# Kernel optimization log

Hardware: AMD Instinct MI355X
Metric: run time of the kernel (lower is better)

The kernel has to match this reference:

```python
import jax, jax.numpy as jnp
import numpy as np

EPS = 1e-12

def _l2_normalize(v, axis):
    norm = jnp.linalg.norm(v, ord=2, axis=axis, keepdims=True)
    return v / jnp.maximum(norm, EPS)

def setup_inputs() -> dict:
    key = jax.random.key(0)
    k1, k2, k3 = jax.random.split(key, 3)
    B, H, W, D, K = 16, 56, 56, 512, 32
    x = jax.random.normal(k1, (B, H, W, D), dtype=jnp.float32)
    # 1x1 conv weight (no bias): equivalent to a (D,K) matmul; he_normal-ish scale
    Wc = jax.random.normal(k2, (D, K), dtype=jnp.float32) * jnp.sqrt(2.0 / D)
    # cluster centers, original shape (1,1,1,512,32) -> stored as (D,K)
    C = jax.random.normal(k3, (D, K), dtype=jnp.float32) * jnp.sqrt(2.0 / D)
    return {"x": x, "Wc": Wc, "C": C}

def reference(x, Wc, C):
    # soft-assignment: 1x1 conv + softmax over clusters
    s = jnp.einsum('bhwd,dk->bhwk', x, Wc)          # (B,H,W,K)
    a = jax.nn.softmax(s, axis=-1)                   # (B,H,W,K)
    # v[b,d,k] = sum_{h,w} a[b,h,w,k] * (x[b,h,w,d] + C[d,k])
    #          = einsum(a,x) + C * sum_{h,w} a   (avoids (B,H,W,D,K) intermediate)
    ax = jnp.einsum('bhwk,bhwd->bdk', a, x)          # (B,D,K)
    a_sum = jnp.sum(a, axis=(1, 2))                  # (B,K)
    v = ax + C[None, :, :] * a_sum[:, None, :]       # (B,D,K)
    # intra-normalize over cluster axis (dim=2), flatten, L2 normalize
    v = _l2_normalize(v, axis=2)
    v = v.reshape(v.shape[0], -1)                    # (B, D*K)
    return _l2_normalize(v, axis=1)
```

## Files before the change

kernel.cpp:

```cpp
#include <hip/hip_runtime.h>
#include <math.h>


#define BATCH 16
#define HW    3136
#define DIM   512
#define KCL   32
#define NCHK  49
#define SLABF (BATCH * DIM * KCL + 256)

typedef __attribute__((ext_vector_type(8))) short short8;
typedef __attribute__((ext_vector_type(4))) float f32x4;

__device__ __forceinline__ void atomAddF(float* p, float v) {
    unsafeAtomicAdd(p, v);
}

__device__ __forceinline__ unsigned short f2bf(float f) {
    unsigned u = __float_as_uint(f);
    return (unsigned short)((u + 0x7FFFu + ((u >> 16) & 1u)) >> 16);
}

__device__ __forceinline__ short8 pack_frag(float4 lo, float4 hi) {
    union { unsigned short h[8]; short8 s; } r;
    r.h[0] = f2bf(lo.x); r.h[1] = f2bf(lo.y); r.h[2] = f2bf(lo.z); r.h[3] = f2bf(lo.w);
    r.h[4] = f2bf(hi.x); r.h[5] = f2bf(hi.y); r.h[6] = f2bf(hi.z); r.h[7] = f2bf(hi.w);
    return r.s;
}

#define WT_STR 520
#define AT_STR 72
#define XT_STR 72

#define LOAD_PF(PF, DC)                                                        \
    _Pragma("unroll")                                                          \
    for (int i = 0; i < 8; ++i) {                                              \
        const int p = (ph + 2 * i) * 4;                                        \
        _Pragma("unroll")                                                      \
        for (int j = 0; j < 4; ++j)                                            \
            PF[i * 4 + j] = xc[(size_t)(p + j) * DIM + (DC)];                  \
    }

#define P2_STAGE(PF)                                                           \
    _Pragma("unroll")                                                          \
    for (int i = 0; i < 8; ++i) {                                              \
        const int p = (ph + 2 * i) * 4;                                        \
        ushort4 w;                                                             \
        w.x = f2bf(PF[i * 4 + 0]); w.y = f2bf(PF[i * 4 + 1]);                  \
        w.z = f2bf(PF[i * 4 + 2]); w.w = f2bf(PF[i * 4 + 3]);                  \
        *(ushort4*)&xt[xtrow * XT_STR + (p ^ xsw)] = w;                        \
    }

#define P2_MFMA_STORE(DC)                                                      \
    {                                                                          \
        f32x4 z = {0.f, 0.f, 0.f, 0.f};                                        \
        f32x4 pacc[2][2];                                                      \
        pacc[0][0] = z; pacc[0][1] = z; pacc[1][0] = z; pacc[1][1] = z;        \
        _Pragma("unroll")                                                      \
        for (int s_ = 0; s_ < 2; ++s_) {                                       \
            const int pb = s_ * 32 + quad * 8;                                 \
            short8 bf0 = *(const short8*)&aT[l15 * AT_STR + pb];               \
            short8 bf1 = *(const short8*)&aT[(16 + l15) * AT_STR + pb];        \
            _Pragma("unroll")                                                  \
            for (int m2 = 0; m2 < 2; ++m2) {                                   \
                const int dloc = wv * 32 + m2 * 16 + l15;                      \
                short8 af = *(const short8*)&xt[dloc * XT_STR + (pb ^ (((dloc >> 3) & 7) << 3))]; \
                pacc[m2][0] = __builtin_amdgcn_mfma_f32_16x16x32_bf16(af, bf0, pacc[m2][0], 0, 0, 0); \
                pacc[m2][1] = __builtin_amdgcn_mfma_f32_16x16x32_bf16(af, bf1, pacc[m2][1], 0, 0, 0); \
            }                                                                  \
        }                                                                      \
        _Pragma("unroll")                                                      \
        for (int m2 = 0; m2 < 2; ++m2) {                                       \
            const int dr = (DC) + (wv * 2 + m2) * 16 + quad * 4;               \
            _Pragma("unroll")                                                  \
            for (int r = 0; r < 4; ++r) {                                      \
                vp[(size_t)(dr + r) * KCL + l15]      = pacc[m2][0][r];        \
                vp[(size_t)(dr + r) * KCL + 16 + l15] = pacc[m2][1][r];        \
            }                                                                  \
        }                                                                      \
    }

__global__ __launch_bounds__(256, 3) void k_sax(const float* __restrict__ x,
                                                const float* __restrict__ Wc,
                                                float* __restrict__ vpart,
                                                float* __restrict__ a_sum) {
    __shared__ __align__(16) unsigned short wt[32 * WT_STR];
    __shared__ __align__(16) unsigned short aT[KCL * AT_STR];
    __shared__ float asum_l[4][32];
    const int t    = threadIdx.x;
    const int lane = t & 63;
    const int wv   = t >> 6;
    const int l15  = lane & 15;
    const int quad = lane >> 4;
    const int n0   = blockIdx.x * 64;
    const int b    = n0 / HW;
    const int ch   = blockIdx.x % NCHK;

    const float* xr = x + (size_t)(n0 + wv * 16 + l15) * DIM + quad * 8;

    float4 afb[2][2];
#pragma unroll
    for (int c = 0; c < 2; ++c) {
        afb[c][0] = *(const float4*)(xr + c * 32);
        afb[c][1] = *(const float4*)(xr + c * 32 + 4);
    }

#pragma unroll
    for (int i = 0; i < 16; ++i) {
        int f  = i * 256 + t;
        int d  = f >> 3;
        int k4 = (f & 7) * 4;
        float4 v = *(const float4*)(Wc + (size_t)d * KCL + k4);
        wt[(k4 + 0) * WT_STR + d] = f2bf(v.x);
        wt[(k4 + 1) * WT_STR + d] = f2bf(v.y);
        wt[(k4 + 2) * WT_STR + d] = f2bf(v.z);
        wt[(k4 + 3) * WT_STR + d] = f2bf(v.w);
    }
    __syncthreads();

    f32x4 acc0 = {0.f, 0.f, 0.f, 0.f};
    f32x4 acc1 = {0.f, 0.f, 0.f, 0.f};
#pragma unroll
    for (int c = 0; c < 16; ++c) {
        float4 lo = afb[c & 1][0], hi = afb[c & 1][1];
        if (c < 14) {
            afb[c & 1][0] = *(const float4*)(xr + (c + 2) * 32);
            afb[c & 1][1] = *(const float4*)(xr + (c + 2) * 32 + 4);
        }
        short8 af = pack_frag(lo, hi);
        short8 b0 = *(const short8*)&wt[l15 * WT_STR + c * 32 + quad * 8];
        short8 b1 = *(const short8*)&wt[(16 + l15) * WT_STR + c * 32 + quad * 8];
        acc0 = __builtin_amdgcn_mfma_f32_16x16x32_bf16(af, b0, acc0, 0, 0, 0);
        acc1 = __builtin_amdgcn_mfma_f32_16x16x32_bf16(af, b1, acc1, 0, 0, 0);
    }

    float at0 = 0.f, at1 = 0.f;
#pragma unroll
    for (int r = 0; r < 4; ++r) {
        float m = fmaxf(acc0[r], acc1[r]);
        m = fmaxf(m, __shfl_xor(m, 1));
        m = fmaxf(m, __shfl_xor(m, 2));
        m = fmaxf(m, __shfl_xor(m, 4));
        m = fmaxf(m, __shfl_xor(m, 8));
        float e0 = __expf(acc0[r] - m);
        float e1 = __expf(acc1[r] - m);
        float s = e0 + e1;
        s += __shfl_xor(s, 1);
        s += __shfl_xor(s, 2);
        s += __shfl_xor(s, 4);
        s += __shfl_xor(s, 8);
        float inv = 1.f / s;
        float a0 = e0 * inv, a1 = e1 * inv;
        const int pos = wv * 16 + quad * 4 + r;
        aT[l15 * AT_STR + pos]        = f2bf(a0);
        aT[(16 + l15) * AT_STR + pos] = f2bf(a1);
        at0 += a0; at1 += a1;
    }
    at0 += __shfl_xor(at0, 16); at0 += __shfl_xor(at0, 32);
    at1 += __shfl_xor(at1, 16); at1 += __shfl_xor(at1, 32);
    if (quad == 0) {
        asum_l[wv][l15]      = at0;
        asum_l[wv][16 + l15] = at1;
    }

    const int rw    = lane & 31;
    const int ph    = lane >> 5;
    const int xtrow = wv * 32 + rw;
    const int xsw   = ((xtrow >> 3) & 7) << 3;
    unsigned short* xt = wt;
    const float* xc = x + (size_t)n0 * DIM + xtrow;
    float* vp = vpart + (size_t)ch * SLABF + (size_t)b * DIM * KCL;

    float pfA[32], pfB[32];
    LOAD_PF(pfA, 0);

    __syncthreads();
    if (t < 32)
        atomAddF(&a_sum[b * KCL + t],
                 asum_l[0][t] + asum_l[1][t] + asum_l[2][t] + asum_l[3][t]);

    LOAD_PF(pfB, 128);

    P2_STAGE(pfA);
    __syncthreads();
    LOAD_PF(pfA, 256);
    P2_MFMA_STORE(0);
    P2_STAGE(pfB);
    __syncthreads();
    LOAD_PF(pfB, 384);
    P2_MFMA_STORE(128);
    P2_STAGE(pfA);
    __syncthreads();
    P2_MFMA_STORE(256);
    P2_STAGE(pfB);
    __syncthreads();
    P2_MFMA_STORE(384);
}

__global__ __launch_bounds__(256) void k_norm1(const float* __restrict__ vpart,
                                               const float* __restrict__ a_sum,
                                               const float* __restrict__ Cc,
                                               float* __restrict__ out,
                                               float* __restrict__ ssq) {
    const int t = threadIdx.x;
    const int row = blockIdx.x * 8 + (t >> 5);
    const int k = t & 31;
    const int b = row >> 9;
    const int d = row & 511;

    const float* vp = vpart + (size_t)row * KCL + k;
    float s0 = 0.f, s1 = 0.f, s2 = 0.f, s3 = 0.f;
#pragma unroll
    for (int ps = 0; ps < 48; ps += 4) {
        s0 += vp[(size_t)(ps + 0) * SLABF];
        s1 += vp[(size_t)(ps + 1) * SLABF];
        s2 += vp[(size_t)(ps + 2) * SLABF];
        s3 += vp[(size_t)(ps + 3) * SLABF];
    }
    s0 += vp[(size_t)48 * SLABF];
    float v = (s0 + s1) + (s2 + s3) + Cc[d * KCL + k] * a_sum[b * KCL + k];

    float ss = v * v;
    ss += __shfl_xor(ss, 1, 32);  ss += __shfl_xor(ss, 2, 32);
    ss += __shfl_xor(ss, 4, 32);  ss += __shfl_xor(ss, 8, 32);
    ss += __shfl_xor(ss, 16, 32);
    float inv = 1.f / fmaxf(sqrtf(ss), 1e-12f);
    float r = v * inv;
    out[(size_t)row * KCL + k] = r;

    float bs = r * r;
    for (int off = 32; off > 0; off >>= 1) bs += __shfl_down(bs, off, 64);
    __shared__ float red[4];
    if ((t & 63) == 0) red[t >> 6] = bs;
    __syncthreads();
    if (t == 0) atomAddF(&ssq[b], (red[0] + red[1]) + (red[2] + red[3]));
}

__global__ __launch_bounds__(256) void k_norm2(float* __restrict__ out,
                                               const float* __restrict__ ssq) {
    const int i4 = blockIdx.x * 256 + threadIdx.x;
    const int b = i4 >> 12;
    float inv = 1.f / fmaxf(sqrtf(ssq[b]), 1e-12f);
    float4 v = *(float4*)(out + (size_t)i4 * 4);
    v.x *= inv; v.y *= inv; v.z *= inv; v.w *= inv;
    *(float4*)(out + (size_t)i4 * 4) = v;
}

extern "C" void kernel_launch(void* const* d_in, const int* in_sizes, int n_in,
                              void* d_out, int out_size, void* d_ws, size_t ws_size,
                              hipStream_t stream) {
    const float* x  = (const float*)d_in[0];
    const float* Wc = (const float*)d_in[1];
    const float* Cc = (const float*)d_in[2];
    float* out = (float*)d_out;

    char* ws = (char*)d_ws;
    float* vpart = (float*)ws;
    float* a_sum = (float*)(ws + (size_t)NCHK * SLABF * 4);
    float* ssq   = (float*)(ws + (size_t)NCHK * SLABF * 4 + 2048);

    hipMemsetAsync(a_sum, 0, 2048 + 64, stream);

    k_sax  <<<784, 256, 0, stream>>>(x, Wc, vpart, a_sum);
    k_norm1<<<1024, 256, 0, stream>>>(vpart, a_sum, Cc, out, ssq);
    k_norm2<<<256, 256, 0, stream>>>(out, ssq);
}
```

Before: 198.2 us.

## Deepen x prefetch with asm loads and explicit vmcnt waits, drop phase-2 barriers

Phase 1 now issues eight chunks of x loads up front through inline-asm global loads. It consumes them with explicitly counted vmcnt waits, so memory latency overlaps the MFMA chain. Phase 2 drops its block-wide barriers between the staging and MFMA steps and uses explicit vmcnt waits to keep more prefetched loads in flight. The a_sum atomic moves to the end of the kernel. The deeper prefetch raises register pressure. Removing the barriers is only safe if each wave reads back only the shared-memory rows it wrote itself.

```diff
diff --git a/kernel.cpp b/kernel.cpp
--- a/kernel.cpp
+++ b/kernel.cpp
@@ -21,24 +21,52 @@
     return (unsigned short)((u + 0x7FFFu + ((u >> 16) & 1u)) >> 16);
 }
 
-__device__ __forceinline__ short8 pack_frag(float4 lo, float4 hi) {
+__device__ __forceinline__ short8 pack_frag(f32x4 lo, f32x4 hi) {
     union { unsigned short h[8]; short8 s; } r;
-    r.h[0] = f2bf(lo.x); r.h[1] = f2bf(lo.y); r.h[2] = f2bf(lo.z); r.h[3] = f2bf(lo.w);
-    r.h[4] = f2bf(hi.x); r.h[5] = f2bf(hi.y); r.h[6] = f2bf(hi.z); r.h[7] = f2bf(hi.w);
+    r.h[0] = f2bf(lo[0]); r.h[1] = f2bf(lo[1]); r.h[2] = f2bf(lo[2]); r.h[3] = f2bf(lo[3]);
+    r.h[4] = f2bf(hi[0]); r.h[5] = f2bf(hi[1]); r.h[6] = f2bf(hi[2]); r.h[7] = f2bf(hi[3]);
     return r.s;
 }
+
+__device__ __forceinline__ f32x4 gload4(const float* p) {
+    f32x4 r;
+    asm volatile("global_load_dwordx4 %0, %1, off" : "=v"(r) : "v"(p) : "memory");
+    return r;
+}
+__device__ __forceinline__ float gload1(const float* p) {
+    float r;
+    asm volatile("global_load_dword %0, %1, off" : "=v"(r) : "v"(p) : "memory");
+    return r;
+}
+
+#define WAITV(N)                                                               \
+    do {                                                                       \
+        asm volatile("s_waitcnt vmcnt(" #N ")" ::: "memory");                  \
+        __builtin_amdgcn_sched_barrier(0);                                     \
+    } while (0)
 
 #define WT_STR 520
 #define AT_STR 72
 #define XT_STR 72
 
-#define LOAD_PF(PF, DC)                                                        \
+#define P1_TAIL(C, N)                                                          \
+    {                                                                          \
+        asm volatile("s_waitcnt vmcnt(" #N ")" ::: "memory");                  \
+        __builtin_amdgcn_sched_barrier(0);                                     \
+        short8 af = pack_frag(afb[(C) & 7][0], afb[(C) & 7][1]);               \
+        short8 b0 = *(const short8*)&wt[l15 * WT_STR + (C) * 32 + quad * 8];   \
+        short8 b1 = *(const short8*)&wt[(16 + l15) * WT_STR + (C) * 32 + quad * 8]; \
+        acc0 = __builtin_amdgcn_mfma_f32_16x16x32_bf16(af, b0, acc0, 0, 0, 0); \
+        acc1 = __builtin_amdgcn_mfma_f32_16x16x32_bf16(af, b1, acc1, 0, 0, 0); \
+    }
+
+#define LOAD_PF_ASM(PF, DC)                                                    \
     _Pragma("unroll")                                                          \
     for (int i = 0; i < 8; ++i) {                                              \
         const int p = (ph + 2 * i) * 4;                                        \
         _Pragma("unroll")                                                      \
         for (int j = 0; j < 4; ++j)                                            \
-            PF[i * 4 + j] = xc[(size_t)(p + j) * DIM + (DC)];                  \
+            PF[i * 4 + j] = gload1(xc + (size_t)(p + j) * DIM + (DC));         \
     }
 
 #define P2_STAGE(PF)                                                           \
@@ -98,11 +126,11 @@
 
     const float* xr = x + (size_t)(n0 + wv * 16 + l15) * DIM + quad * 8;
 
-    float4 afb[2][2];
-#pragma unroll
-    for (int c = 0; c < 2; ++c) {
-        afb[c][0] = *(const float4*)(xr + c * 32);
-        afb[c][1] = *(const float4*)(xr + c * 32 + 4);
+    f32x4 afb[8][2];
+#pragma unroll
+    for (int c = 0; c < 8; ++c) {
+        afb[c][0] = gload4(xr + c * 32);
+        afb[c][1] = gload4(xr + c * 32 + 4);
     }
 
 #pragma unroll
@@ -117,22 +145,22 @@
         wt[(k4 + 3) * WT_STR + d] = f2bf(v.w);
     }
     __syncthreads();
+    WAITV(0);
 
     f32x4 acc0 = {0.f, 0.f, 0.f, 0.f};
     f32x4 acc1 = {0.f, 0.f, 0.f, 0.f};
 #pragma unroll
-    for (int c = 0; c < 16; ++c) {
-        float4 lo = afb[c & 1][0], hi = afb[c & 1][1];
-        if (c < 14) {
-            afb[c & 1][0] = *(const float4*)(xr + (c + 2) * 32);
-            afb[c & 1][1] = *(const float4*)(xr + (c + 2) * 32 + 4);
-        }
-        short8 af = pack_frag(lo, hi);
+    for (int c = 0; c < 8; ++c) {
+        short8 af = pack_frag(afb[c][0], afb[c][1]);
+        afb[c][0] = gload4(xr + (c + 8) * 32);
+        afb[c][1] = gload4(xr + (c + 8) * 32 + 4);
         short8 b0 = *(const short8*)&wt[l15 * WT_STR + c * 32 + quad * 8];
         short8 b1 = *(const short8*)&wt[(16 + l15) * WT_STR + c * 32 + quad * 8];
         acc0 = __builtin_amdgcn_mfma_f32_16x16x32_bf16(af, b0, acc0, 0, 0, 0);
         acc1 = __builtin_amdgcn_mfma_f32_16x16x32_bf16(af, b1, acc1, 0, 0, 0);
     }
+    P1_TAIL(8, 14)  P1_TAIL(9, 12)  P1_TAIL(10, 10) P1_TAIL(11, 8)
+    P1_TAIL(12, 6)  P1_TAIL(13, 4)  P1_TAIL(14, 2)  P1_TAIL(15, 0)
 
     float at0 = 0.f, at1 = 0.f;
 #pragma unroll
@@ -172,29 +200,29 @@
     float* vp = vpart + (size_t)ch * SLABF + (size_t)b * DIM * KCL;
 
     float pfA[32], pfB[32];
-    LOAD_PF(pfA, 0);
+    LOAD_PF_ASM(pfA, 0);
 
     __syncthreads();
+
+    WAITV(0);
+    LOAD_PF_ASM(pfB, 128);
+    P2_STAGE(pfA);
+    P2_MFMA_STORE(0);
+    LOAD_PF_ASM(pfA, 256);
+    WAITV(48);
+    P2_STAGE(pfB);
+    P2_MFMA_STORE(128);
+    LOAD_PF_ASM(pfB, 384);
+    WAITV(48);
+    P2_STAGE(pfA);
+    P2_MFMA_STORE(256);
+    WAITV(16);
+    P2_STAGE(pfB);
+    P2_MFMA_STORE(384);
+
     if (t < 32)
         atomAddF(&a_sum[b * KCL + t],
                  asum_l[0][t] + asum_l[1][t] + asum_l[2][t] + asum_l[3][t]);
-
-    LOAD_PF(pfB, 128);
-
-    P2_STAGE(pfA);
-    __syncthreads();
-    LOAD_PF(pfA, 256);
-    P2_MFMA_STORE(0);
-    P2_STAGE(pfB);
-    __syncthreads();
-    LOAD_PF(pfB, 384);
-    P2_MFMA_STORE(128);
-    P2_STAGE(pfA);
-    __syncthreads();
-    P2_MFMA_STORE(256);
-    P2_STAGE(pfB);
-    __syncthreads();
-    P2_MFMA_STORE(384);
 }
 
 __global__ __launch_bounds__(256) void k_norm1(const float* __restrict__ vpart,
```

Result: no change. 196.2 us (-1.0%).
